# Kernel tuning notes

Hardware: AMD Instinct MI355X
Metric: run time of the kernel (lower is better)

## Reference

```python
import jax, jax.numpy as jnp
import numpy as np

B, S, H, NH = 4, 2048, 1024, 16
D = H // NH  # d_per_head = 64


def setup_inputs() -> dict:
    key = jax.random.key(0)
    ks = jax.random.split(key, 6)
    return {
        "x": jax.random.normal(ks[0], (B, S, H), dtype=jnp.float32),
        "W_query": jax.random.uniform(ks[1], (NH, D, H), dtype=jnp.float32),
        "W_key": jax.random.uniform(ks[2], (NH, D, H), dtype=jnp.float32),
        "W_value": jax.random.uniform(ks[3], (NH, D, H), dtype=jnp.float32),
        "W_out": jax.random.normal(ks[4], (H, H), dtype=jnp.float32) * 0.02,
        "b_out": jnp.zeros((H,), dtype=jnp.float32),
    }


def reference(x, W_query, W_key, W_value, W_out, b_out):
    b, s, h = x.shape
    n_head, d, _ = W_query.shape
    # ALiBi: slope_i = -(i+1); distance[q, k] = k - q (non-causal, full softmax)
    dist = (jnp.arange(s)[None, :] - jnp.arange(s)[:, None]).astype(x.dtype)  # [s, s]
    slopes = -(jnp.arange(1, n_head + 1, dtype=x.dtype))  # [n_head]
    # per-head projections: x @ W[i].T  -> [b, n, s, d]
    q = jnp.einsum("bsh,ndh->bnsd", x, W_query)
    k = jnp.einsum("bsh,ndh->bnsd", x, W_key)
    v = jnp.einsum("bsh,ndh->bnsd", x, W_value)
    scores = jnp.einsum("bnqd,bnkd->bnqk", q, k) / jnp.sqrt(jnp.asarray(d, x.dtype))
    scores = scores + slopes[None, :, None, None] * dist[None, None, :, :]
    attn = jax.nn.softmax(scores, axis=-1)
    heads = jnp.einsum("bnqk,bnkd->bnqd", attn, v)  # [b, n, s, d]
    # concat heads along feature dim (head 0 first, matching torch cat order)
    multi = heads.transpose(0, 2, 1, 3).reshape(b, s, n_head * d)
    return multi @ W_out.T + b_out
```

## Files before the change

### kernel.cpp

```cpp
#include <hip/hip_runtime.h>
#include <hip/hip_bf16.h>
#include <stdint.h>

typedef unsigned short u16;
typedef short bf16x8 __attribute__((ext_vector_type(8)));
typedef float f32x4 __attribute__((ext_vector_type(4)));
typedef uint32_t u32x4 __attribute__((ext_vector_type(4)));

#define DEV __device__ __forceinline__

DEV u16 f2bf(float f) {
  union { float f; uint32_t u; } v; v.f = f;
  uint32_t u = v.u;
  return (u16)((u + 0x7FFFu + ((u >> 16) & 1u)) >> 16);
}
DEV float bf2f(u16 h) {
  union { uint32_t u; float f; } v; v.u = ((uint32_t)h) << 16;
  return v.f;
}
DEV uint32_t cvtpk_bf16(float lo, float hi) {
  uint32_t r;
  asm volatile("v_cvt_pk_bf16_f32 %0, %1, %2" : "=v"(r) : "v"(lo), "v"(hi));
  return r;
}

#if __has_builtin(__builtin_amdgcn_exp2f)
#define EXP2F(x) __builtin_amdgcn_exp2f(x)
#else
#define EXP2F(x) exp2f(x)
#endif

#define GLL(gp, lp) __builtin_amdgcn_global_load_lds(\
    (const __attribute__((address_space(1))) unsigned int*)(gp), \
    (__attribute__((address_space(3))) unsigned int*)(lp), 16, 0, 0)

__global__ void prep_x(const float* __restrict__ x, u16* __restrict__ xh, u16* __restrict__ xl) {
  int i = blockIdx.x * 256 + threadIdx.x;
  float4 v = ((const float4*)x)[i];
  ushort4 h, lo;
  h.x = f2bf(v.x); h.y = f2bf(v.y); h.z = f2bf(v.z); h.w = f2bf(v.w);
  lo.x = f2bf(v.x - bf2f(h.x)); lo.y = f2bf(v.y - bf2f(h.y));
  lo.z = f2bf(v.z - bf2f(h.z)); lo.w = f2bf(v.w - bf2f(h.w));
  ((ushort4*)xh)[i] = h;
  ((ushort4*)xl)[i] = lo;
}

__global__ void prep_w(const float* __restrict__ wq, const float* __restrict__ wk,
                       const float* __restrict__ wv, const float* __restrict__ wo,
                       u16* __restrict__ wqkh, u16* __restrict__ wqkl,
                       u16* __restrict__ wvb, u16* __restrict__ wob) {
  int i = blockIdx.x * 256 + threadIdx.x;
  int seg = i >> 18;
  int j = i & ((1 << 18) - 1);
  const float* src = (seg == 0) ? wq : (seg == 1) ? wk : (seg == 2) ? wv : wo;
  float4 v = ((const float4*)src)[j];
  ushort4 h;
  h.x = f2bf(v.x); h.y = f2bf(v.y); h.z = f2bf(v.z); h.w = f2bf(v.w);
  if (seg < 2) {
    ushort4 lo;
    lo.x = f2bf(v.x - bf2f(h.x)); lo.y = f2bf(v.y - bf2f(h.y));
    lo.z = f2bf(v.z - bf2f(h.z)); lo.w = f2bf(v.w - bf2f(h.w));
    ((ushort4*)wqkh)[i] = h;
    ((ushort4*)wqkl)[i] = lo;
  } else if (seg == 2) {
    ((ushort4*)wvb)[j] = h;
  } else {
    ((ushort4*)wob)[j] = h;
  }
}

__global__ __launch_bounds__(256, 2) void qkv_gemm(
    const u16* __restrict__ xh, const u16* __restrict__ xl,
    const u16* __restrict__ wh, const u16* __restrict__ wl,
    const u16* __restrict__ wv,
    u16* __restrict__ qkh, u16* __restrict__ qkl, u16* __restrict__ vout) {
  __shared__ u16 Ah[128 * 32], Al[128 * 32], Bh[128 * 32], Bl[128 * 32];
  const int t = threadIdx.x, w = t >> 6, l = t & 63, g = l >> 4, lr = l & 15;
  const int m0 = blockIdx.y * 128, n0 = blockIdx.x * 128;
  const bool split = (n0 < 2048);
  const u16* bsrc_h = split ? (wh + (size_t)n0 * 1024) : (wv + (size_t)(n0 - 2048) * 1024);
  const u16* bsrc_l = split ? (wl + (size_t)n0 * 1024) : wl;
  const int wr = w >> 1, wc = w & 1;

  f32x4 zero = {0.f, 0.f, 0.f, 0.f};
  f32x4 acc[4][4];
#pragma unroll
  for (int mi = 0; mi < 4; ++mi)
#pragma unroll
    for (int ni = 0; ni < 4; ++ni) acc[mi][ni] = zero;

  for (int k0 = 0; k0 < 1024; k0 += 32) {
    __syncthreads();
#pragma unroll
    for (int i = 0; i < 2; ++i) {
      const int c = i * 256 + t;
      const int row = c >> 2;
      const int kc8 = (c & 3) * 8;
      const size_t goff = (size_t)row * 1024 + k0 + kc8;
      const int lo = i * 4096 + w * 1024;
      GLL(xh + (size_t)m0 * 1024 + goff, (char*)Ah + lo);
      GLL(bsrc_h + goff, (char*)Bh + lo);
      if (split) {
        GLL(xl + (size_t)m0 * 1024 + goff, (char*)Al + lo);
        GLL(bsrc_l + goff, (char*)Bl + lo);
      }
    }
    __syncthreads();

    bf16x8 ah[4], al[4];
#pragma unroll
    for (int mi = 0; mi < 4; ++mi) {
      const int idx = (wr * 64 + mi * 16 + lr) * 32 + g * 8;
      ah[mi] = *(const bf16x8*)&Ah[idx];
      if (split) al[mi] = *(const bf16x8*)&Al[idx];
    }
#pragma unroll
    for (int ni = 0; ni < 4; ++ni) {
      const int idx = (wc * 64 + ni * 16 + lr) * 32 + g * 8;
      bf16x8 bh = *(const bf16x8*)&Bh[idx];
      bf16x8 bl;
      if (split) bl = *(const bf16x8*)&Bl[idx];
#pragma unroll
      for (int mi = 0; mi < 4; ++mi) {
        acc[mi][ni] = __builtin_amdgcn_mfma_f32_16x16x32_bf16(ah[mi], bh, acc[mi][ni], 0, 0, 0);
        if (split) {
          acc[mi][ni] = __builtin_amdgcn_mfma_f32_16x16x32_bf16(al[mi], bh, acc[mi][ni], 0, 0, 0);
          acc[mi][ni] = __builtin_amdgcn_mfma_f32_16x16x32_bf16(ah[mi], bl, acc[mi][ni], 0, 0, 0);
        }
      }
    }
  }

#pragma unroll
  for (int mi = 0; mi < 4; ++mi)
#pragma unroll
    for (int ni = 0; ni < 4; ++ni)
#pragma unroll
      for (int r = 0; r < 4; ++r) {
        const int row = m0 + wr * 64 + mi * 16 + g * 4 + r;
        const int col = wc * 64 + ni * 16 + lr;
        const float cval = acc[mi][ni][r];
        if (split) {
          const u16 h = f2bf(cval);
          qkh[(size_t)row * 2048 + n0 + col] = h;
          qkl[(size_t)row * 2048 + n0 + col] = f2bf(cval - bf2f(h));
        } else {
          vout[(size_t)row * 1024 + (n0 - 2048) + col] = f2bf(cval);
        }
      }
}

__global__ __launch_bounds__(256) void vtrans(const u16* __restrict__ vin, u16* __restrict__ vout) {
  __shared__ u16 Ts[64 * 66];
  const int t = threadIdx.x;
  const int r0 = blockIdx.y * 64, c0 = blockIdx.x * 64;
  const int rl = t >> 3, cc = (t & 7) * 8;
#pragma unroll
  for (int i = 0; i < 2; ++i) {
    const int r = rl + i * 32;
    bf16x8 v = *(const bf16x8*)&vin[(size_t)(r0 + r) * 1024 + c0 + cc];
#pragma unroll
    for (int e = 0; e < 8; ++e) Ts[(cc + e) * 66 + r] = (u16)v[e];
  }
  __syncthreads();
  const int c = t >> 2, seg = (t & 3) * 16;
  u16 tmp[16];
#pragma unroll
  for (int e = 0; e < 16; ++e) tmp[e] = Ts[c * 66 + seg + e];
  *(bf16x8*)&vout[(size_t)(c0 + c) * 8192 + r0 + seg] = *(const bf16x8*)&tmp[0];
  *(bf16x8*)&vout[(size_t)(c0 + c) * 8192 + r0 + seg + 8] = *(const bf16x8*)&tmp[8];
}

__global__ __launch_bounds__(512, 2) void attn(
    const u16* __restrict__ qkh, const u16* __restrict__ qkl,
    const u16* __restrict__ vt, u16* __restrict__ multi) {
  __shared__ u16 Ksh[2][4096], Ksl[2][4096], Vts[2][4096];
  const int t = threadIdx.x, w = t >> 6, l = t & 63, g = l >> 4, lr = l & 15;
  const int L = blockIdx.x;
  const int flat = (L & 7) * 64 + (L >> 3);
  const int b = flat >> 7, h = (flat >> 3) & 15, qt = flat & 7;
  const int q0 = qt * 256;
  const size_t rowbase = (size_t)b * 2048;
  const u16* Qh = qkh + rowbase * 2048 + h * 64;
  const u16* Ql = qkl + rowbase * 2048 + h * 64;
  const u16* Kh = qkh + rowbase * 2048 + 1024 + h * 64;
  const u16* Kl = qkl + rowbase * 2048 + 1024 + h * 64;
  const u16* Vb = vt + (size_t)(h * 64) * 8192 + b * 2048;

  const int srow = l >> 3;
  const int sj = (l & 7) ^ srow;
  const int krow = w * 8 + srow;
  const int klog = ((krow >> 5) << 5) | (((krow >> 2) & 3) << 3)
                 | (((krow >> 4) & 1) << 2) | (krow & 3);
  const int ldsoff = w * 1024;

  bf16x8 qfh[2][2], qfl[2][2];
#pragma unroll
  for (int nt = 0; nt < 2; ++nt)
#pragma unroll
    for (int kc = 0; kc < 2; ++kc) {
      const size_t off = (size_t)(q0 + w * 32 + nt * 16 + lr) * 2048 + kc * 32 + g * 8;
      qfh[nt][kc] = *(const bf16x8*)&Qh[off];
      qfl[nt][kc] = *(const bf16x8*)&Ql[off];
    }

  f32x4 zero = {0.f, 0.f, 0.f, 0.f};
  f32x4 o[2][4];
#pragma unroll
  for (int nt = 0; nt < 2; ++nt)
#pragma unroll
    for (int dn = 0; dn < 4; ++dn) o[nt][dn] = zero;
  float mst[2] = {-3.0e38f, -3.0e38f};
  float lst[2] = {0.f, 0.f};

  const float c1 = 0.125f * 1.44269504088896f;
  const float slope2 = -(float)(h + 1) * 1.44269504088896f;
  const float s2r1 = slope2, s2r2 = slope2 * 2.0f, s2r3 = slope2 * 3.0f;
  float base[4];
#pragma unroll
  for (int mt = 0; mt < 4; ++mt)
    base[mt] = slope2 * (float)(((mt >> 1) << 5) + ((mt & 1) << 2) + g * 8);
  const float bstep = slope2 * 64.0f;

  GLL(Kh + (size_t)klog * 2048 + sj * 8, (char*)&Ksh[0][0] + ldsoff);
  GLL(Kl + (size_t)klog * 2048 + sj * 8, (char*)&Ksl[0][0] + ldsoff);
  GLL(Vb + (size_t)krow * 8192 + sj * 8, (char*)&Vts[0][0] + ldsoff);
  __syncthreads();

  int cur = 0;
  for (int kt = 0; kt < 2048; kt += 64) {
    if (kt + 64 < 2048) {
      const int nxt = cur ^ 1;
      GLL(Kh + (size_t)(kt + 64 + klog) * 2048 + sj * 8, (char*)&Ksh[nxt][0] + ldsoff);
      GLL(Kl + (size_t)(kt + 64 + klog) * 2048 + sj * 8, (char*)&Ksl[nxt][0] + ldsoff);
      GLL(Vb + (size_t)krow * 8192 + kt + 64 + sj * 8, (char*)&Vts[nxt][0] + ldsoff);
    }
    const u16* Kcur = &Ksh[cur][0];
    const u16* Lcur = &Ksl[cur][0];
    const u16* Vcur = &Vts[cur][0];

    f32x4 c[4][2];
#pragma unroll
    for (int mt = 0; mt < 4; ++mt)
#pragma unroll
      for (int nt = 0; nt < 2; ++nt) c[mt][nt] = zero;
    __builtin_amdgcn_s_setprio(1);
#pragma unroll
    for (int mt = 0; mt < 4; ++mt) {
      bf16x8 ah[2], al[2];
#pragma unroll
      for (int kc = 0; kc < 2; ++kc) {
        const int rk = mt * 16 + lr;
        const int byte = rk * 128 + (((kc * 4 + g) ^ (rk & 7)) << 4);
        ah[kc] = *(const bf16x8*)((const char*)Kcur + byte);
        al[kc] = *(const bf16x8*)((const char*)Lcur + byte);
      }
#pragma unroll
      for (int nt = 0; nt < 2; ++nt) {
        f32x4 a = c[mt][nt];
        a = __builtin_amdgcn_mfma_f32_16x16x32_bf16(ah[0], qfh[nt][0], a, 0, 0, 0);
        a = __builtin_amdgcn_mfma_f32_16x16x32_bf16(ah[1], qfh[nt][1], a, 0, 0, 0);
        a = __builtin_amdgcn_mfma_f32_16x16x32_bf16(al[0], qfh[nt][0], a, 0, 0, 0);
        a = __builtin_amdgcn_mfma_f32_16x16x32_bf16(al[1], qfh[nt][1], a, 0, 0, 0);
        a = __builtin_amdgcn_mfma_f32_16x16x32_bf16(ah[0], qfl[nt][0], a, 0, 0, 0);
        a = __builtin_amdgcn_mfma_f32_16x16x32_bf16(ah[1], qfl[nt][1], a, 0, 0, 0);
        c[mt][nt] = a;
      }
    }
    __builtin_amdgcn_s_setprio(0);

#pragma unroll
    for (int mt = 0; mt < 4; ++mt)
#pragma unroll
      for (int nt = 0; nt < 2; ++nt) {
        f32x4 a = c[mt][nt];
        a[0] = fmaf(a[0], c1, base[mt]);
        a[1] = fmaf(a[1], c1, base[mt] + s2r1);
        a[2] = fmaf(a[2], c1, base[mt] + s2r2);
        a[3] = fmaf(a[3], c1, base[mt] + s2r3);
        c[mt][nt] = a;
      }
    float rmax[2];
#pragma unroll
    for (int nt = 0; nt < 2; ++nt) {
      float m01 = fmaxf(fmaxf(c[0][nt][0], c[0][nt][1]), fmaxf(c[0][nt][2], c[0][nt][3]));
      float m23 = fmaxf(fmaxf(c[1][nt][0], c[1][nt][1]), fmaxf(c[1][nt][2], c[1][nt][3]));
      float m45 = fmaxf(fmaxf(c[2][nt][0], c[2][nt][1]), fmaxf(c[2][nt][2], c[2][nt][3]));
      float m67 = fmaxf(fmaxf(c[3][nt][0], c[3][nt][1]), fmaxf(c[3][nt][2], c[3][nt][3]));
      float m = fmaxf(fmaxf(m01, m23), fmaxf(m45, m67));
      m = fmaxf(m, __shfl_xor(m, 16));
      m = fmaxf(m, __shfl_xor(m, 32));
      rmax[nt] = m;
    }
    const bool need = (rmax[0] > mst[0]) | (rmax[1] > mst[1]);
    if (__any(need)) {
#pragma unroll
      for (int nt = 0; nt < 2; ++nt) {
        const float mn = fmaxf(mst[nt], rmax[nt]);
        const float alpha = EXP2F(mst[nt] - mn);
        mst[nt] = mn;
        lst[nt] *= alpha;
#pragma unroll
        for (int dn = 0; dn < 4; ++dn) {
          o[nt][dn][0] *= alpha; o[nt][dn][1] *= alpha;
          o[nt][dn][2] *= alpha; o[nt][dn][3] *= alpha;
        }
      }
    }
    bf16x8 pb[2][2];
#pragma unroll
    for (int nt = 0; nt < 2; ++nt) {
      float rsum = 0.f;
      uint32_t pk01[4], pk23[4];
#pragma unroll
      for (int mt = 0; mt < 4; ++mt) {
        const float p0 = EXP2F(c[mt][nt][0] - mst[nt]);
        const float p1 = EXP2F(c[mt][nt][1] - mst[nt]);
        const float p2 = EXP2F(c[mt][nt][2] - mst[nt]);
        const float p3 = EXP2F(c[mt][nt][3] - mst[nt]);
        rsum += (p0 + p1) + (p2 + p3);
        pk01[mt] = cvtpk_bf16(p0, p1);
        pk23[mt] = cvtpk_bf16(p2, p3);
      }
      rsum += __shfl_xor(rsum, 16);
      rsum += __shfl_xor(rsum, 32);
      lst[nt] += rsum;
      union { u32x4 u; bf16x8 bf; } cv0, cv1;
      cv0.u = (u32x4){pk01[0], pk23[0], pk01[1], pk23[1]};
      cv1.u = (u32x4){pk01[2], pk23[2], pk01[3], pk23[3]};
      pb[nt][0] = cv0.bf;
      pb[nt][1] = cv1.bf;
    }

    __builtin_amdgcn_s_setprio(1);
#pragma unroll
    for (int dn = 0; dn < 4; ++dn) {
      bf16x8 vb[2];
#pragma unroll
      for (int kc = 0; kc < 2; ++kc) {
        const int row = dn * 16 + lr;
        const int jk = kc * 4 + g;
        const int byte = row * 128 + ((jk ^ (row & 7)) << 4);
        vb[kc] = *(const bf16x8*)((const char*)Vcur + byte);
      }
#pragma unroll
      for (int nt = 0; nt < 2; ++nt) {
        o[nt][dn] = __builtin_amdgcn_mfma_f32_16x16x32_bf16(vb[0], pb[nt][0], o[nt][dn], 0, 0, 0);
        o[nt][dn] = __builtin_amdgcn_mfma_f32_16x16x32_bf16(vb[1], pb[nt][1], o[nt][dn], 0, 0, 0);
      }
    }
    __builtin_amdgcn_s_setprio(0);

#pragma unroll
    for (int mt = 0; mt < 4; ++mt) base[mt] += bstep;

    __syncthreads();
    cur ^= 1;
  }

#pragma unroll
  for (int nt = 0; nt < 2; ++nt) {
    const float rinv = 1.0f / lst[nt];
    const int qrow = q0 + w * 32 + nt * 16 + lr;
#pragma unroll
    for (int dn = 0; dn < 4; ++dn) {
      uint2 pkv;
      pkv.x = cvtpk_bf16(o[nt][dn][0] * rinv, o[nt][dn][1] * rinv);
      pkv.y = cvtpk_bf16(o[nt][dn][2] * rinv, o[nt][dn][3] * rinv);
      *(uint2*)&multi[(rowbase + qrow) * 1024 + h * 64 + dn * 16 + g * 4] = pkv;
    }
  }
}

__global__ __launch_bounds__(256, 2) void out_gemm(
    const u16* __restrict__ A, const u16* __restrict__ Bw,
    const float* __restrict__ bias, float* __restrict__ out) {
  __shared__ u16 As[128 * 32], Bs[128 * 32];
  const int t = threadIdx.x, w = t >> 6, l = t & 63, g = l >> 4, lr = l & 15;
  const int m0 = blockIdx.y * 128, n0 = blockIdx.x * 128;
  const int wr = w >> 1, wc = w & 1;

  f32x4 zero = {0.f, 0.f, 0.f, 0.f};
  f32x4 acc[4][4];
#pragma unroll
  for (int mi = 0; mi < 4; ++mi)
#pragma unroll
    for (int ni = 0; ni < 4; ++ni) acc[mi][ni] = zero;

  for (int k0 = 0; k0 < 1024; k0 += 32) {
    __syncthreads();
#pragma unroll
    for (int i = 0; i < 2; ++i) {
      const int c = i * 256 + t;
      const int row = c >> 2;
      const int kc8 = (c & 3) * 8;
      const size_t goff = (size_t)row * 1024 + k0 + kc8;
      const int lo = i * 4096 + w * 1024;
      GLL(A + (size_t)m0 * 1024 + goff, (char*)As + lo);
      GLL(Bw + (size_t)n0 * 1024 + goff, (char*)Bs + lo);
    }
    __syncthreads();

    bf16x8 ah[4];
#pragma unroll
    for (int mi = 0; mi < 4; ++mi)
      ah[mi] = *(const bf16x8*)&As[(wr * 64 + mi * 16 + lr) * 32 + g * 8];
#pragma unroll
    for (int ni = 0; ni < 4; ++ni) {
      bf16x8 bh = *(const bf16x8*)&Bs[(wc * 64 + ni * 16 + lr) * 32 + g * 8];
#pragma unroll
      for (int mi = 0; mi < 4; ++mi)
        acc[mi][ni] = __builtin_amdgcn_mfma_f32_16x16x32_bf16(ah[mi], bh, acc[mi][ni], 0, 0, 0);
    }
  }

#pragma unroll
  for (int mi = 0; mi < 4; ++mi)
#pragma unroll
    for (int ni = 0; ni < 4; ++ni)
#pragma unroll
      for (int r = 0; r < 4; ++r) {
        const int row = m0 + wr * 64 + mi * 16 + g * 4 + r;
        const int col = n0 + wc * 64 + ni * 16 + lr;
        out[(size_t)row * 1024 + col] = acc[mi][ni][r] + bias[col];
      }
}

extern "C" void kernel_launch(void* const* d_in, const int* in_sizes, int n_in,
                              void* d_out, int out_size, void* d_ws, size_t ws_size,
                              hipStream_t stream) {
  (void)in_sizes; (void)n_in; (void)out_size; (void)ws_size;
  const float* x  = (const float*)d_in[0];
  const float* wq = (const float*)d_in[1];
  const float* wk = (const float*)d_in[2];
  const float* wv = (const float*)d_in[3];
  const float* wo = (const float*)d_in[4];
  const float* bo = (const float*)d_in[5];
  float* out = (float*)d_out;
  char* ws = (char*)d_ws;

  const size_t MB = 1024 * 1024;
  u16* xh   = (u16*)(ws + 0);
  u16* xl   = (u16*)(ws + 16 * MB);
  u16* qkh  = (u16*)(ws + 32 * MB);
  u16* qkl  = (u16*)(ws + 64 * MB);
  u16* vbf  = (u16*)(ws + 96 * MB);
  u16* wqkh = (u16*)(ws + 112 * MB);
  u16* wqkl = (u16*)(ws + 116 * MB);
  u16* wvb  = (u16*)(ws + 120 * MB);
  u16* wob  = (u16*)(ws + 122 * MB);
  u16* multi = xh;
  u16* vt    = xl;

  prep_x<<<8192, 256, 0, stream>>>(x, xh, xl);
  prep_w<<<4096, 256, 0, stream>>>(wq, wk, wv, wo, wqkh, wqkl, wvb, wob);
  qkv_gemm<<<dim3(24, 64), 256, 0, stream>>>(xh, xl, wqkh, wqkl, wvb, qkh, qkl, vbf);
  vtrans<<<dim3(16, 128), 256, 0, stream>>>(vbf, vt);
  attn<<<512, 512, 0, stream>>>(qkh, qkl, vt, multi);
  out_gemm<<<dim3(8, 64), 256, 0, stream>>>(multi, wob, bo, out);
}
```

Measured before the change: 347.5 us.

## Triple-buffer K/V tiles and software-pipeline QK with softmax-PV

Moves the attention kernel from double to triple LDS buffering and splits each iteration into QK, softmax+PV and staging lambdas. The loop is unrolled by two so that the QK MFMAs for the next tile are issued before the softmax and PV of the current tile. This is meant to overlap matrix work with the exp and reduction work and to hide global-to-LDS load latency. In exchange, LDS use per block grows to about 72KB and a second score accumulator stays live, which raises register pressure and may reduce occupancy at two blocks per CU.

```diff
diff --git a/kernel.cpp b/kernel.cpp
--- a/kernel.cpp
+++ b/kernel.cpp
@@ -174,7 +174,7 @@
 __global__ __launch_bounds__(512, 2) void attn(
     const u16* __restrict__ qkh, const u16* __restrict__ qkl,
     const u16* __restrict__ vt, u16* __restrict__ multi) {
-  __shared__ u16 Ksh[2][4096], Ksl[2][4096], Vts[2][4096];
+  __shared__ u16 Ksh[3][4096], Ksl[3][4096], Vts[3][4096];
   const int t = threadIdx.x, w = t >> 6, l = t & 63, g = l >> 4, lr = l & 15;
   const int L = blockIdx.x;
   const int flat = (L & 7) * 64 + (L >> 3);
@@ -222,24 +222,15 @@
     base[mt] = slope2 * (float)(((mt >> 1) << 5) + ((mt & 1) << 2) + g * 8);
   const float bstep = slope2 * 64.0f;
 
-  GLL(Kh + (size_t)klog * 2048 + sj * 8, (char*)&Ksh[0][0] + ldsoff);
-  GLL(Kl + (size_t)klog * 2048 + sj * 8, (char*)&Ksl[0][0] + ldsoff);
-  GLL(Vb + (size_t)krow * 8192 + sj * 8, (char*)&Vts[0][0] + ldsoff);
-  __syncthreads();
-
-  int cur = 0;
-  for (int kt = 0; kt < 2048; kt += 64) {
-    if (kt + 64 < 2048) {
-      const int nxt = cur ^ 1;
-      GLL(Kh + (size_t)(kt + 64 + klog) * 2048 + sj * 8, (char*)&Ksh[nxt][0] + ldsoff);
-      GLL(Kl + (size_t)(kt + 64 + klog) * 2048 + sj * 8, (char*)&Ksl[nxt][0] + ldsoff);
-      GLL(Vb + (size_t)krow * 8192 + kt + 64 + sj * 8, (char*)&Vts[nxt][0] + ldsoff);
-    }
-    const u16* Kcur = &Ksh[cur][0];
-    const u16* Lcur = &Ksl[cur][0];
-    const u16* Vcur = &Vts[cur][0];
-
-    f32x4 c[4][2];
+  auto STAGE = [&](int tile, int buf) {
+    GLL(Kh + (size_t)(tile * 64 + klog) * 2048 + sj * 8, (char*)&Ksh[buf][0] + ldsoff);
+    GLL(Kl + (size_t)(tile * 64 + klog) * 2048 + sj * 8, (char*)&Ksl[buf][0] + ldsoff);
+    GLL(Vb + (size_t)krow * 8192 + tile * 64 + sj * 8, (char*)&Vts[buf][0] + ldsoff);
+  };
+
+  auto QK = [&](int buf, f32x4 (&c)[4][2]) {
+    const u16* Kcur = &Ksh[buf][0];
+    const u16* Lcur = &Ksl[buf][0];
 #pragma unroll
     for (int mt = 0; mt < 4; ++mt)
 #pragma unroll
@@ -268,7 +259,10 @@
       }
     }
     __builtin_amdgcn_s_setprio(0);
-
+  };
+
+  auto SMPV = [&](f32x4 (&c)[4][2], int buf) {
+    const u16* Vcur = &Vts[buf][0];
 #pragma unroll
     for (int mt = 0; mt < 4; ++mt)
 #pragma unroll
@@ -292,8 +286,8 @@
       m = fmaxf(m, __shfl_xor(m, 32));
       rmax[nt] = m;
     }
-    const bool need = (rmax[0] > mst[0]) | (rmax[1] > mst[1]);
-    if (__any(need)) {
+    const bool needr = (rmax[0] > mst[0]) | (rmax[1] > mst[1]);
+    if (__any(needr)) {
 #pragma unroll
       for (int nt = 0; nt < 2; ++nt) {
         const float mn = fmaxf(mst[nt], rmax[nt]);
@@ -331,7 +325,6 @@
       pb[nt][0] = cv0.bf;
       pb[nt][1] = cv1.bf;
     }
-
     __builtin_amdgcn_s_setprio(1);
 #pragma unroll
     for (int dn = 0; dn < 4; ++dn) {
@@ -350,13 +343,29 @@
       }
     }
     __builtin_amdgcn_s_setprio(0);
-
 #pragma unroll
     for (int mt = 0; mt < 4; ++mt) base[mt] += bstep;
-
-    __syncthreads();
-    cur ^= 1;
-  }
+  };
+
+  STAGE(0, 0);
+  STAGE(1, 1);
+  __syncthreads();
+  f32x4 cA[4][2], cB[4][2];
+  QK(0, cA);
+
+  for (int kt = 0; kt < 30; kt += 2) {
+    STAGE(kt + 2, (kt + 2) % 3);
+    QK((kt + 1) % 3, cB);
+    SMPV(cA, kt % 3);
+    __syncthreads();
+    STAGE(kt + 3, (kt + 3) % 3);
+    QK((kt + 2) % 3, cA);
+    SMPV(cB, (kt + 1) % 3);
+    __syncthreads();
+  }
+  QK(31 % 3, cB);
+  SMPV(cA, 30 % 3);
+  SMPV(cB, 31 % 3);
 
 #pragma unroll
   for (int nt = 0; nt < 2; ++nt) {
```

Result: no change. 343.5 us (-1.1%).
